# Optimization experiments

Hardware: AMD Instinct MI355X
Metric: run time of the kernel (lower is better)

Reference implementation:

```python
import jax, jax.numpy as jnp
import numpy as np

B, N, C, H = 2, 2048, 1024, 16
D = C // H  # head dim = 64
SCALE = 1.0 / np.sqrt(D)
BASE = 10000.0  # ntk_factor=1.0 => base unchanged


def setup_inputs() -> dict:
    key = jax.random.key(0)
    k1, k2, k3, k4 = jax.random.split(key, 4)
    x = jax.random.normal(k1, (B, N, C), dtype=jnp.float32)
    Wqkv = jax.random.normal(k2, (C, 3 * C), dtype=jnp.float32) * (1.0 / np.sqrt(C))
    Wout = jax.random.normal(k3, (C, C), dtype=jnp.float32) * (1.0 / np.sqrt(C))
    bout = jax.random.normal(k4, (C,), dtype=jnp.float32) * 0.01
    return {"x": x, "Wqkv": Wqkv, "Wout": Wout, "bout": bout}


def _rope_tables(n, d, dtype):
    inv_freq = 1.0 / (BASE ** (jnp.arange(0, d, 2, dtype=jnp.float32) / d))
    t = jnp.arange(n, dtype=jnp.float32)
    freqs = t[:, None] * inv_freq[None, :]            # [N, D/2]
    cos = jnp.cos(freqs)[None, :, None, :].astype(dtype)  # [1,N,1,D/2]
    sin = jnp.sin(freqs)[None, :, None, :].astype(dtype)
    return cos, sin


def _apply_rope(u, cos, sin):
    # u: [B,N,H,D]; strided-halves RoPE variant (cat, not interleave)
    u1, u2 = u[..., ::2], u[..., 1::2]
    return jnp.concatenate([u1 * cos - u2 * sin, u1 * sin + u2 * cos], axis=-1)


def reference(x, Wqkv, Wout, bout):
    b, n, c = x.shape
    qkv = (x @ Wqkv).reshape(b, n, 3, H, D)
    q, k, v = qkv[:, :, 0], qkv[:, :, 1], qkv[:, :, 2]  # [B,N,H,D]
    cos, sin = _rope_tables(n, D, x.dtype)
    q = _apply_rope(q, cos, sin)
    k = _apply_rope(k, cos, sin)
    scores = jnp.einsum("bqhd,bkhd->bhqk", q, k) * SCALE
    causal = jnp.triu(jnp.ones((n, n), dtype=bool), k=1)
    scores = jnp.where(causal, -jnp.inf, scores)
    attn = jax.nn.softmax(scores, axis=-1)
    out = jnp.einsum("bhqk,bkhd->bqhd", attn, v).reshape(b, n, c)
    return out @ Wout + bout
```

## Files before the change

kernel.cpp:

```cpp
#include <hip/hip_runtime.h>
#include <hip/hip_bf16.h>
#include <math.h>

#define B_ 2
#define N_ 2048
#define C_ 1024
#define H_ 16
#define D_ 64
#define M_ 4096
#define QKV_N 3072
#define SCALE_ 0.125f
#define FIXM 8.0f

typedef unsigned short u16;
typedef unsigned int u32;
using bf16x8   = __attribute__((ext_vector_type(8))) __bf16;
using ushortx8 = __attribute__((ext_vector_type(8))) unsigned short;
using floatx4  = __attribute__((ext_vector_type(4))) float;

__device__ __forceinline__ float bf2f(u16 u) {
    union { u32 i; float f; } v; v.i = ((u32)u) << 16; return v.f;
}
__device__ __forceinline__ u16 f2bf(float f) {
    union { float f; u32 i; } v; v.f = f;
    u32 r = (v.i + 0x7fff + ((v.i >> 16) & 1)) >> 16;
    return (u16)r;
}
__device__ __forceinline__ u32 pk2bf(float a, float b) {
    __hip_bfloat162 h = __float22bfloat162_rn(make_float2(a, b));
    union { __hip_bfloat162 h; u32 u; } c; c.h = h; return c.u;
}

__device__ __forceinline__ void gl2lds16(const void* g, void* l) {
    __builtin_amdgcn_global_load_lds(
        (const __attribute__((address_space(1))) unsigned int*)(unsigned long long)g,
        (__attribute__((address_space(3))) unsigned int*)(unsigned long long)l,
        16, 0, 0);
}

__constant__ unsigned char UQI[24] = {7,15,15,14,14,6,13,13,12,12,5,11,11,10,10,4,9,9,8,8,3,2,1,0};
__constant__ unsigned char UT0[24] = {0,0,16,0,15,0,0,14,0,13,0,0,12,0,11,0,0,10,0,9,0,0,0,0};
__constant__ unsigned char UNT[24] = {16,16,16,15,15,14,14,14,13,13,12,12,12,11,11,10,10,10,9,9,8,6,4,2};

__device__ __forceinline__ void do_convtrans(const float* W, u16* Wt, int K, int N,
                                             int nb, int kb, int tid) {
    int n = nb * 256 + tid;
    int k0 = kb * 128;
    #pragma unroll
    for (int kk = 0; kk < 128; kk += 8) {
        ushortx8 v;
        #pragma unroll
        for (int j = 0; j < 8; j++)
            v[j] = f2bf(W[(size_t)(k0 + kk + j) * N + n]);
        *(ushortx8*)(&Wt[(size_t)n * K + k0 + kk]) = v;
    }
}

__global__ __launch_bounds__(256) void prep_kernel(
    const float* __restrict__ x, const float* __restrict__ Wqkv,
    float* __restrict__ cosT, float* __restrict__ sinT,
    u16* __restrict__ xb, u16* __restrict__ Wqkvt)
{
    int bid = blockIdx.x, tid = threadIdx.x;
    if (bid < 2048) {
        int i = bid * 256 + tid;
        const float4* p = (const float4*)x + (size_t)i * 2;
        float4 a = p[0], b = p[1];
        ushortx8 v;
        v[0] = f2bf(a.x); v[1] = f2bf(a.y); v[2] = f2bf(a.z); v[3] = f2bf(a.w);
        v[4] = f2bf(b.x); v[5] = f2bf(b.y); v[6] = f2bf(b.z); v[7] = f2bf(b.w);
        *(ushortx8*)(xb + (size_t)i * 8) = v;
    } else if (bid < 2304) {
        int idx = (bid - 2048) * 256 + tid;
        int n = idx >> 5, i = idx & 31;
        double inv = pow(10000.0, -(double)i / 32.0);
        double f = (double)n * inv;
        cosT[idx] = (float)cos(f);
        sinT[idx] = (float)sin(f);
    } else {
        int u = bid - 2304;
        do_convtrans(Wqkv, Wqkvt, C_, QKV_N, u % 12, u / 12, tid);
    }
}

__global__ __launch_bounds__(256) void wout_trans(const float* __restrict__ Wout,
                                                  u16* __restrict__ Woutt) {
    do_convtrans(Wout, Woutt, C_, C_, blockIdx.x % 4, blockIdx.x / 4, threadIdx.x);
}

__global__ __launch_bounds__(256) void gemm128(
    const u16* __restrict__ A, const u16* __restrict__ Bt,
    void* __restrict__ Cm, const float* __restrict__ bias, int fp32out,
    int M, int N, int K)
{
    __shared__ u16 As[128 * 32];
    __shared__ u16 Bs[128 * 32];
    const int t = threadIdx.x;
    const int w = t >> 6, lane = t & 63;
    const int quad = lane >> 4, cc = lane & 15;
    const int m0 = blockIdx.y * 128, n0 = blockIdx.x * 128;
    const int wm = (w >> 1) * 64, wn = (w & 1) * 64;

    floatx4 acc[4][4];
    floatx4 zero = {0.f, 0.f, 0.f, 0.f};
    #pragma unroll
    for (int i = 0; i < 4; i++)
        #pragma unroll
        for (int j = 0; j < 4; j++) acc[i][j] = zero;

    const int srow = lane >> 2, skof = (lane & 3) * 8;

    for (int k0 = 0; k0 < K; k0 += 32) {
        __syncthreads();
        #pragma unroll
        for (int c = 0; c < 2; c++) {
            int chunk = w * 2 + c;
            int row = chunk * 16 + srow;
            gl2lds16(A  + (size_t)(m0 + row) * K + k0 + skof, (char*)As + chunk * 1024);
            gl2lds16(Bt + (size_t)(n0 + row) * K + k0 + skof, (char*)Bs + chunk * 1024);
        }
        __syncthreads();

        bf16x8 af[4], bf[4];
        #pragma unroll
        for (int i = 0; i < 4; i++)
            af[i] = *(const bf16x8*)(&As[(wm + i * 16 + cc) * 32 + quad * 8]);
        #pragma unroll
        for (int j = 0; j < 4; j++)
            bf[j] = *(const bf16x8*)(&Bs[(wn + j * 16 + cc) * 32 + quad * 8]);
        #pragma unroll
        for (int i = 0; i < 4; i++)
            #pragma unroll
            for (int j = 0; j < 4; j++)
                acc[i][j] = __builtin_amdgcn_mfma_f32_16x16x32_bf16(af[i], bf[j], acc[i][j], 0, 0, 0);
    }

    #pragma unroll
    for (int i = 0; i < 4; i++)
        #pragma unroll
        for (int j = 0; j < 4; j++)
            #pragma unroll
            for (int r = 0; r < 4; r++) {
                int row = m0 + wm + i * 16 + quad * 4 + r;
                int col = n0 + wn + j * 16 + cc;
                float v = acc[i][j][r];
                if (fp32out) ((float*)Cm)[(size_t)row * N + col] = v + bias[col];
                else         ((u16*)Cm)[(size_t)row * N + col] = f2bf(v);
            }
}

__global__ void rope_kernel(const u16* __restrict__ qkv,
                            const float* __restrict__ cosT, const float* __restrict__ sinT,
                            u16* __restrict__ Qh, u16* __restrict__ Kh, u16* __restrict__ Vh)
{
    int idx = blockIdx.x * 256 + threadIdx.x;
    if (idx >= B_ * N_ * H_ * 32) return;
    int i = idx & 31;
    int h = (idx >> 5) & (H_ - 1);
    int n = (idx >> 9) & (N_ - 1);
    int b = idx >> 20;
    size_t m = (size_t)b * N_ + n;
    const u16* row = qkv + m * QKV_N;
    float cs = cosT[n * 32 + i], sn = sinT[n * 32 + i];

    float q1 = bf2f(row[h * 64 + 2 * i]),      q2 = bf2f(row[h * 64 + 2 * i + 1]);
    float k1 = bf2f(row[C_ + h * 64 + 2 * i]), k2 = bf2f(row[C_ + h * 64 + 2 * i + 1]);
    size_t obase = ((size_t)(b * H_ + h) * N_ + n) * D_;
    Qh[obase + i]      = f2bf((q1 * cs - q2 * sn) * SCALE_);
    Qh[obase + 32 + i] = f2bf((q1 * sn + q2 * cs) * SCALE_);
    Kh[obase + i]      = f2bf(k1 * cs - k2 * sn);
    Kh[obase + 32 + i] = f2bf(k1 * sn + k2 * cs);
    Vh[obase + 2 * i]     = row[2 * C_ + h * 64 + 2 * i];
    Vh[obase + 2 * i + 1] = row[2 * C_ + h * 64 + 2 * i + 1];
}

__global__ __launch_bounds__(256) void attn_kernel(
    const u16* __restrict__ Qh, const u16* __restrict__ Kh,
    const u16* __restrict__ Vh, u16* __restrict__ Ao,
    float* __restrict__ Opart, float* __restrict__ lpart)
{
    constexpr int LDK = 66;
    __shared__ u16 Ks[2][64 * LDK];
    __shared__ u16 Vs[2][64 * LDK];
    __shared__ u16 Ps[4 * 32 * LDK];

    const int t = threadIdx.x;
    const int wave = t >> 6, lane = t & 63;
    const int quad = lane >> 4, cc = lane & 15;
    const int u = blockIdx.x;
    const int qi = UQI[u], tile0 = UT0[u], ntl = UNT[u];
    const int qb0 = qi * 128;
    const int bh = blockIdx.y;
    const size_t hb = (size_t)bh * N_ * D_;

    bf16x8 qf[2][2];
    #pragma unroll
    for (int qt = 0; qt < 2; qt++) {
        const u16* qrow = Qh + hb + (size_t)(qb0 + qt * 64 + wave * 16 + cc) * D_;
        qf[qt][0] = *(const bf16x8*)(qrow + quad * 8);
        qf[qt][1] = *(const bf16x8*)(qrow + 32 + quad * 8);
    }

    floatx4 zero = {0.f, 0.f, 0.f, 0.f};
    floatx4 Oacc[2][4];
    float lsum[2] = {0.f, 0.f};
    #pragma unroll
    for (int qt = 0; qt < 2; qt++)
        #pragma unroll
        for (int j = 0; j < 4; j++) Oacc[qt][j] = zero;

    const int krow = t >> 3, kch = (t & 7) * 8;
    const int kp = t >> 3, vchunk = (t & 7) * 8;
    const int qlocal = wave * 16 + cc;
    u32* psd = (u32*)Ps;

    bf16x8 kr[2]; ushortx8 vr[2];
    {
        int kb = tile0 * 64;
        kr[0] = *(const bf16x8*)(Kh + hb + (size_t)(kb + krow) * D_ + kch);
        kr[1] = *(const bf16x8*)(Kh + hb + (size_t)(kb + krow + 32) * D_ + kch);
        vr[0] = *(const ushortx8*)(Vh + hb + (size_t)(kb + 2 * kp) * D_ + vchunk);
        vr[1] = *(const ushortx8*)(Vh + hb + (size_t)(kb + 2 * kp + 1) * D_ + vchunk);
    }

    for (int ti = 0; ti < ntl; ti++) {
        const int kb = (tile0 + ti) * 64;
        const int c = ti & 1;
        *(bf16x8*)(&Ks[c][krow * LDK + kch]) = kr[0];
        *(bf16x8*)(&Ks[c][(krow + 32) * LDK + kch]) = kr[1];
        u32* vsd = (u32*)Vs[c];
        #pragma unroll
        for (int e = 0; e < 8; e++)
            vsd[(vchunk + e) * 33 + kp] = (u32)vr[0][e] | ((u32)vr[1][e] << 16);
        if (ti + 1 < ntl) {
            int kb2 = (tile0 + ti + 1) * 64;
            kr[0] = *(const bf16x8*)(Kh + hb + (size_t)(kb2 + krow) * D_ + kch);
            kr[1] = *(const bf16x8*)(Kh + hb + (size_t)(kb2 + krow + 32) * D_ + kch);
            vr[0] = *(const ushortx8*)(Vh + hb + (size_t)(kb2 + 2 * kp) * D_ + vchunk);
            vr[1] = *(const ushortx8*)(Vh + hb + (size_t)(kb2 + 2 * kp + 1) * D_ + vchunk);
        }
        __syncthreads();

        const bool act0 = (kb <= qb0);

        floatx4 S[2][4];
        #pragma unroll
        for (int nt = 0; nt < 4; nt++) {
            bf16x8 kf0 = *(const bf16x8*)(&Ks[c][(nt * 16 + cc) * LDK + quad * 8]);
            bf16x8 kf1 = *(const bf16x8*)(&Ks[c][(nt * 16 + cc) * LDK + 32 + quad * 8]);
            floatx4 a1 = zero;
            a1 = __builtin_amdgcn_mfma_f32_16x16x32_bf16(kf0, qf[1][0], a1, 0, 0, 0);
            a1 = __builtin_amdgcn_mfma_f32_16x16x32_bf16(kf1, qf[1][1], a1, 0, 0, 0);
            S[1][nt] = a1;
            if (act0) {
                floatx4 a0 = zero;
                a0 = __builtin_amdgcn_mfma_f32_16x16x32_bf16(kf0, qf[0][0], a0, 0, 0, 0);
                a0 = __builtin_amdgcn_mfma_f32_16x16x32_bf16(kf1, qf[0][1], a0, 0, 0, 0);
                S[0][nt] = a0;
            }
        }

        #pragma unroll
        for (int qt = 0; qt < 2; qt++) {
            if (qt == 0 && !act0) continue;
            const bool diag = (kb == qb0 + qt * 64);
            const int prow = (wave * 32 + qt * 16 + cc) * 33;
            #pragma unroll
            for (int nt = 0; nt < 4; nt++) {
                float p[4];
                #pragma unroll
                for (int r = 0; r < 4; r++) {
                    int key_l = nt * 16 + quad * 4 + r;
                    float e = __expf(S[qt][nt][r] - FIXM);
                    p[r] = (diag && (key_l > qlocal)) ? 0.0f : e;
                    lsum[qt] += p[r];
                }
                psd[prow + nt * 8 + quad * 2]     = pk2bf(p[0], p[1]);
                psd[prow + nt * 8 + quad * 2 + 1] = pk2bf(p[2], p[3]);
            }
        }

        #pragma unroll
        for (int s = 0; s < 2; s++) {
            bf16x8 pf1 = *(const bf16x8*)(&Ps[(wave * 32 + 16 + cc) * LDK + s * 32 + quad * 8]);
            bf16x8 pf0;
            if (act0) pf0 = *(const bf16x8*)(&Ps[(wave * 32 + cc) * LDK + s * 32 + quad * 8]);
            #pragma unroll
            for (int j = 0; j < 4; j++) {
                bf16x8 vf = *(const bf16x8*)(&Vs[c][(j * 16 + cc) * LDK + s * 32 + quad * 8]);
                Oacc[1][j] = __builtin_amdgcn_mfma_f32_16x16x32_bf16(pf1, vf, Oacc[1][j], 0, 0, 0);
                if (act0)
                    Oacc[0][j] = __builtin_amdgcn_mfma_f32_16x16x32_bf16(pf0, vf, Oacc[0][j], 0, 0, 0);
            }
        }
    }

    const bool partial = (qi >= 8);
    const int cid = (tile0 > 0) ? 1 : 0;
    const int slot = ((bh * 8 + (qi - 8)) * 2 + cid);
    const int b = bh >> 4, h = bh & (H_ - 1);

    #pragma unroll
    for (int qt = 0; qt < 2; qt++) {
        float lf = lsum[qt];
        lf += __shfl_xor(lf, 16, 64);
        lf += __shfl_xor(lf, 32, 64);
        if (!partial) {
            #pragma unroll
            for (int r = 0; r < 4; r++) {
                float l_r = __shfl(lf, quad * 4 + r, 64);
                float inv = 1.0f / l_r;
                int n = qb0 + qt * 64 + wave * 16 + quad * 4 + r;
                #pragma unroll
                for (int j = 0; j < 4; j++)
                    Ao[((size_t)b * N_ + n) * C_ + h * D_ + j * 16 + cc] = f2bf(Oacc[qt][j][r] * inv);
            }
        } else {
            #pragma unroll
            for (int r = 0; r < 4; r++) {
                int lrow = qt * 64 + wave * 16 + quad * 4 + r;
                float* Ob = Opart + (size_t)slot * (128 * 64) + (size_t)lrow * 64;
                #pragma unroll
                for (int j = 0; j < 4; j++)
                    Ob[j * 16 + cc] = Oacc[qt][j][r];
            }
            if (lane < 16)
                lpart[slot * 128 + qt * 64 + wave * 16 + cc] = lf;
        }
    }
}

__global__ __launch_bounds__(256) void attn_combine(
    const float* __restrict__ Opart, const float* __restrict__ lpart,
    u16* __restrict__ Ao)
{
    int g = blockIdx.x * 256 + threadIdx.x;
    int f4 = g & 15;
    int row = (g >> 4) & 127;
    int qz = (g >> 11) & 7;
    int bh = g >> 14;
    int s0 = (bh * 8 + qz) * 2;
    const float* O0 = Opart + (size_t)s0 * (128 * 64) + (size_t)row * 64 + f4 * 4;
    const float* O1 = O0 + 128 * 64;
    float l = lpart[s0 * 128 + row] + lpart[(s0 + 1) * 128 + row];
    float inv = 1.0f / l;
    float4 a = *(const float4*)O0, c = *(const float4*)O1;
    int b = bh >> 4, h = bh & (H_ - 1);
    int n = (qz + 8) * 128 + row;
    u16* d = Ao + ((size_t)b * N_ + n) * C_ + h * D_ + f4 * 4;
    d[0] = f2bf((a.x + c.x) * inv);
    d[1] = f2bf((a.y + c.y) * inv);
    d[2] = f2bf((a.z + c.z) * inv);
    d[3] = f2bf((a.w + c.w) * inv);
}

extern "C" void kernel_launch(void* const* d_in, const int* in_sizes, int n_in,
                              void* d_out, int out_size, void* d_ws, size_t ws_size,
                              hipStream_t stream)
{
    const float* x    = (const float*)d_in[0];
    const float* Wqkv = (const float*)d_in[1];
    const float* Wout = (const float*)d_in[2];
    const float* bout = (const float*)d_in[3];

    char* p = (char*)d_ws;
    u16* qkv = (u16*)p; p += (size_t)M_ * QKV_N * 2;
    u16* Qh  = (u16*)p; p += (size_t)B_ * H_ * N_ * D_ * 2;
    u16* Kh  = (u16*)p; p += (size_t)B_ * H_ * N_ * D_ * 2;
    u16* Vh  = (u16*)p; p += (size_t)B_ * H_ * N_ * D_ * 2;
    u16* Ao  = (u16*)p; p += (size_t)M_ * C_ * 2;
    float* cosT = (float*)p; p += (size_t)N_ * 32 * 4;
    float* sinT = (float*)p; p += (size_t)N_ * 32 * 4;

    u16* xb    = Ao;
    u16* Wqkvt = Qh;
    u16* Woutt = qkv;
    float* Opart = (float*)((char*)qkv + (2 << 20));
    float* lpart = (float*)((char*)qkv + (2 << 20) + 512 * 128 * 64 * 4);

    hipLaunchKernelGGL(prep_kernel, dim3(2400), dim3(256), 0, stream,
                       x, Wqkv, cosT, sinT, xb, Wqkvt);
    hipLaunchKernelGGL(gemm128, dim3(QKV_N / 128, M_ / 128), dim3(256), 0, stream,
                       xb, Wqkvt, qkv, (const float*)nullptr, 0, M_, QKV_N, C_);
    hipLaunchKernelGGL(rope_kernel, dim3((B_ * N_ * H_ * 32) / 256), dim3(256), 0, stream,
                       qkv, cosT, sinT, Qh, Kh, Vh);
    hipLaunchKernelGGL(wout_trans, dim3(32), dim3(256), 0, stream, Wout, Woutt);
    hipLaunchKernelGGL(attn_kernel, dim3(24, B_ * H_), dim3(256), 0, stream,
                       Qh, Kh, Vh, Ao, Opart, lpart);
    hipLaunchKernelGGL(attn_combine, dim3((32 * 8 * 128 * 16) / 256), dim3(256), 0, stream,
                       Opart, lpart, Ao);
    hipLaunchKernelGGL(gemm128, dim3(C_ / 128, M_ / 128), dim3(256), 0, stream,
                       Ao, Woutt, d_out, bout, 1, M_, C_, C_);
}
```

Baseline: 229.0 us.

## Split causal attention into finer KV chunks with bf16 partials and fused Wout transpose

Reworks the causal attention work split from 24 to 40 units per head, giving each unit at most 8 KV tiles so later query blocks are split into 2-4 chunks. This evens out per-block work and raises occupancy. Partial outputs are stored in bf16 instead of fp32 to cut combine traffic, and the combine kernel now sums a variable number of chunks. The Wout transpose is folded into the combine launch to save a kernel launch, and the softmax exponent uses exp2f with a fused multiply-add. The cost is more partial writes and combine work, plus some precision loss from rounding the partials to bf16.

```diff
diff --git a/kernel.cpp b/kernel.cpp
--- a/kernel.cpp
+++ b/kernel.cpp
@@ -11,6 +11,7 @@
 #define QKV_N 3072
 #define SCALE_ 0.125f
 #define FIXM 8.0f
+#define L2E 1.442695041f
 
 typedef unsigned short u16;
 typedef unsigned int u32;
@@ -38,9 +39,19 @@
         16, 0, 0);
 }
 
-__constant__ unsigned char UQI[24] = {7,15,15,14,14,6,13,13,12,12,5,11,11,10,10,4,9,9,8,8,3,2,1,0};
-__constant__ unsigned char UT0[24] = {0,0,16,0,15,0,0,14,0,13,0,0,12,0,11,0,0,10,0,9,0,0,0,0};
-__constant__ unsigned char UNT[24] = {16,16,16,15,15,14,14,14,13,13,12,12,12,11,11,10,10,10,9,9,8,6,4,2};
+__constant__ unsigned char UQI[40] = {15,15,15,15,14,14,11,11,11,10,7,7,3,
+                                      14,14,13,13,13,13,12,12,10,10,9,9,6,6,
+                                      12,12,9,8,8,8,5,5,2, 4,4,1,0};
+__constant__ unsigned char UT0[40] = {0,8,16,24,0,8,0,8,16,0,0,8,0,
+                                      16,23,0,7,14,21,0,7,8,15,0,7,0,7,
+                                      14,20,14,0,6,12,0,6,0, 0,5,0,0};
+__constant__ unsigned char UNT[40] = {8,8,8,8,8,8,8,8,8,8,8,8,8,
+                                      7,7,7,7,7,7,7,7,7,7,7,7,7,7,
+                                      6,6,6,6,6,6,6,6,6, 5,5,4,2};
+__constant__ unsigned char UCID[40] = {0,1,2,3,0,1,0,1,2,0,0,1,0,
+                                       2,3,0,1,2,3,0,1,1,2,0,1,0,1,
+                                       2,3,2,0,1,2,0,1,0, 0,1,0,0};
+__constant__ unsigned char SB[16] = {0,0,0,0, 0,2,4,6, 8,11,14,17, 20,24,28,32};
 
 __device__ __forceinline__ void do_convtrans(const float* W, u16* Wt, int K, int N,
                                              int nb, int kb, int tid) {
@@ -83,11 +94,6 @@
     }
 }
 
-__global__ __launch_bounds__(256) void wout_trans(const float* __restrict__ Wout,
-                                                  u16* __restrict__ Woutt) {
-    do_convtrans(Wout, Woutt, C_, C_, blockIdx.x % 4, blockIdx.x / 4, threadIdx.x);
-}
-
 __global__ __launch_bounds__(256) void gemm128(
     const u16* __restrict__ A, const u16* __restrict__ Bt,
     void* __restrict__ Cm, const float* __restrict__ bias, int fp32out,
@@ -177,7 +183,7 @@
 __global__ __launch_bounds__(256) void attn_kernel(
     const u16* __restrict__ Qh, const u16* __restrict__ Kh,
     const u16* __restrict__ Vh, u16* __restrict__ Ao,
-    float* __restrict__ Opart, float* __restrict__ lpart)
+    u16* __restrict__ Opart, float* __restrict__ lpart)
 {
     constexpr int LDK = 66;
     __shared__ u16 Ks[2][64 * LDK];
@@ -188,7 +194,7 @@
     const int wave = t >> 6, lane = t & 63;
     const int quad = lane >> 4, cc = lane & 15;
     const int u = blockIdx.x;
-    const int qi = UQI[u], tile0 = UT0[u], ntl = UNT[u];
+    const int qi = UQI[u], tile0 = UT0[u], ntl = UNT[u], cid = UCID[u];
     const int qb0 = qi * 128;
     const int bh = blockIdx.y;
     const size_t hb = (size_t)bh * N_ * D_;
@@ -271,7 +277,7 @@
                 #pragma unroll
                 for (int r = 0; r < 4; r++) {
                     int key_l = nt * 16 + quad * 4 + r;
-                    float e = __expf(S[qt][nt][r] - FIXM);
+                    float e = exp2f(fmaf(S[qt][nt][r], L2E, -FIXM * L2E));
                     p[r] = (diag && (key_l > qlocal)) ? 0.0f : e;
                     lsum[qt] += p[r];
                 }
@@ -295,9 +301,8 @@
         }
     }
 
-    const bool partial = (qi >= 8);
-    const int cid = (tile0 > 0) ? 1 : 0;
-    const int slot = ((bh * 8 + (qi - 8)) * 2 + cid);
+    const bool partial = (qi >= 4);
+    const int slot = bh * 36 + SB[qi] + cid;
     const int b = bh >> 4, h = bh & (H_ - 1);
 
     #pragma unroll
@@ -319,10 +324,10 @@
             #pragma unroll
             for (int r = 0; r < 4; r++) {
                 int lrow = qt * 64 + wave * 16 + quad * 4 + r;
-                float* Ob = Opart + (size_t)slot * (128 * 64) + (size_t)lrow * 64;
+                u16* Ob = Opart + (size_t)slot * (128 * 64) + (size_t)lrow * 64;
                 #pragma unroll
                 for (int j = 0; j < 4; j++)
-                    Ob[j * 16 + cc] = Oacc[qt][j][r];
+                    Ob[j * 16 + cc] = f2bf(Oacc[qt][j][r]);
             }
             if (lane < 16)
                 lpart[slot * 128 + qt * 64 + wave * 16 + cc] = lf;
@@ -331,27 +336,41 @@
 }
 
 __global__ __launch_bounds__(256) void attn_combine(
-    const float* __restrict__ Opart, const float* __restrict__ lpart,
-    u16* __restrict__ Ao)
-{
+    const u16* __restrict__ Opart, const float* __restrict__ lpart,
+    u16* __restrict__ Ao, const float* __restrict__ Wout, u16* __restrict__ Woutt)
+{
+    if (blockIdx.x >= 3072) {
+        int u = blockIdx.x - 3072;
+        do_convtrans(Wout, Woutt, C_, C_, u % 4, u / 4, threadIdx.x);
+        return;
+    }
     int g = blockIdx.x * 256 + threadIdx.x;
     int f4 = g & 15;
     int row = (g >> 4) & 127;
-    int qz = (g >> 11) & 7;
-    int bh = g >> 14;
-    int s0 = (bh * 8 + qz) * 2;
-    const float* O0 = Opart + (size_t)s0 * (128 * 64) + (size_t)row * 64 + f4 * 4;
-    const float* O1 = O0 + 128 * 64;
-    float l = lpart[s0 * 128 + row] + lpart[(s0 + 1) * 128 + row];
+    int rest = g >> 11;
+    int qq = rest % 12;
+    int bh = rest / 12;
+    int qi = qq + 4;
+    int nch = (qi >= 12) ? 4 : (qi >= 8) ? 3 : 2;
+    int s0 = bh * 36 + SB[qi];
+
+    float o[4] = {0.f, 0.f, 0.f, 0.f};
+    float l = 0.f;
+    for (int cch = 0; cch < nch; cch++) {
+        int slot = s0 + cch;
+        const u16* Ob = Opart + (size_t)slot * (128 * 64) + (size_t)row * 64 + f4 * 4;
+        ushort4 v = *(const ushort4*)Ob;
+        o[0] += bf2f(v.x); o[1] += bf2f(v.y); o[2] += bf2f(v.z); o[3] += bf2f(v.w);
+        l += lpart[slot * 128 + row];
+    }
     float inv = 1.0f / l;
-    float4 a = *(const float4*)O0, c = *(const float4*)O1;
     int b = bh >> 4, h = bh & (H_ - 1);
-    int n = (qz + 8) * 128 + row;
+    int n = qi * 128 + row;
     u16* d = Ao + ((size_t)b * N_ + n) * C_ + h * D_ + f4 * 4;
-    d[0] = f2bf((a.x + c.x) * inv);
-    d[1] = f2bf((a.y + c.y) * inv);
-    d[2] = f2bf((a.z + c.z) * inv);
-    d[3] = f2bf((a.w + c.w) * inv);
+    d[0] = f2bf(o[0] * inv);
+    d[1] = f2bf(o[1] * inv);
+    d[2] = f2bf(o[2] * inv);
+    d[3] = f2bf(o[3] * inv);
 }
 
 extern "C" void kernel_launch(void* const* d_in, const int* in_sizes, int n_in,
@@ -375,8 +394,8 @@
     u16* xb    = Ao;
     u16* Wqkvt = Qh;
     u16* Woutt = qkv;
-    float* Opart = (float*)((char*)qkv + (2 << 20));
-    float* lpart = (float*)((char*)qkv + (2 << 20) + 512 * 128 * 64 * 4);
+    u16* Opart = (u16*)((char*)qkv + ((size_t)2 << 20));
+    float* lpart = (float*)((char*)qkv + ((size_t)21 << 20));
 
     hipLaunchKernelGGL(prep_kernel, dim3(2400), dim3(256), 0, stream,
                        x, Wqkv, cosT, sinT, xb, Wqkvt);
@@ -384,11 +403,10 @@
                        xb, Wqkvt, qkv, (const float*)nullptr, 0, M_, QKV_N, C_);
     hipLaunchKernelGGL(rope_kernel, dim3((B_ * N_ * H_ * 32) / 256), dim3(256), 0, stream,
                        qkv, cosT, sinT, Qh, Kh, Vh);
-    hipLaunchKernelGGL(wout_trans, dim3(32), dim3(256), 0, stream, Wout, Woutt);
-    hipLaunchKernelGGL(attn_kernel, dim3(24, B_ * H_), dim3(256), 0, stream,
+    hipLaunchKernelGGL(attn_kernel, dim3(40, B_ * H_), dim3(256), 0, stream,
                        Qh, Kh, Vh, Ao, Opart, lpart);
-    hipLaunchKernelGGL(attn_combine, dim3((32 * 8 * 128 * 16) / 256), dim3(256), 0, stream,
-                       Opart, lpart, Ao);
+    hipLaunchKernelGGL(attn_combine, dim3(3072 + 32), dim3(256), 0, stream,
+                       Opart, lpart, Ao, Wout, Woutt);
     hipLaunchKernelGGL(gemm128, dim3(C_ / 128, M_ / 128), dim3(256), 0, stream,
                        Ao, Woutt, d_out, bout, 1, M_, C_, C_);
 }
```

Measured after the change: 233.8 us. 1.02x slower.
